# Performance work log

Measured on AMD Instinct MI355X. Metric: run time of the kernel, lower is better.

Reference implementation:

```python
import jax, jax.numpy as jnp
import numpy as np

N = 50000      # nodes
E = 800000     # edges (before self-loops)
F_IN = 256     # feature_size
H = 96         # hidden_channels
G = 64         # graphs in batch
NC = 4         # num_classes
EPS = 1e-5     # BatchNorm eps


def _lrelu(x, s=0.01):
    return jnp.where(x >= 0, x, s * x)


def _gat(x, W, a_s, a_d, b, src, dst):
    # PyG GATConv, heads=1: linear transform, edge-wise LeakyReLU(0.2) scores,
    # segment softmax over destination nodes, scatter-add aggregation.
    h = x @ W                                                  # [N,H]
    e = _lrelu((h * a_s).sum(-1)[src] + (h * a_d).sum(-1)[dst], 0.2)  # [E+N]
    m = jax.ops.segment_max(e, dst, num_segments=N)
    ee = jnp.exp(e - m[dst])
    denom = jax.ops.segment_sum(ee, dst, num_segments=N)
    alpha = ee / denom[dst]
    return jax.ops.segment_sum(alpha[:, None] * h[src], dst, num_segments=N) + b


def _bn(x, g, b):
    # training-mode BatchNorm over the node dimension
    mu = x.mean(0)
    var = ((x - mu) ** 2).mean(0)
    return g * (x - mu) / jnp.sqrt(var + EPS) + b


def setup_inputs() -> dict:
    key = jax.random.key(0)
    ks = jax.random.split(key, 20)
    p = lambda i, sh: jax.random.normal(ks[i], sh, jnp.float32) * 0.05
    inp = {
        "x": jax.random.normal(ks[0], (N, F_IN), jnp.float32),
        "edge_index": jax.random.randint(ks[1], (2, E), 0, N),
        "batch": jnp.sort(jax.random.randint(ks[2], (N,), 0, G)),
        "embed_W": p(3, (F_IN, H)), "embed_b": jnp.zeros((H,), jnp.float32),
        "conv1_W": p(4, (H, H)), "conv1_as": p(5, (H,)), "conv1_ad": p(6, (H,)), "conv1_b": jnp.zeros((H,), jnp.float32),
        "conv2_W": p(7, (H, H)), "conv2_as": p(8, (H,)), "conv2_ad": p(9, (H,)), "conv2_b": jnp.zeros((H,), jnp.float32),
        "conv3_W": p(10, (H, H)), "conv3_as": p(11, (H,)), "conv3_ad": p(12, (H,)), "conv3_b": jnp.zeros((H,), jnp.float32),
        "fc1_W": p(13, (H, H)), "fc1_b": jnp.zeros((H,), jnp.float32),
        "fc2_W": p(14, (H, H)), "fc2_b": jnp.zeros((H,), jnp.float32),
        "bn1_g": jnp.ones((H,), jnp.float32), "bn1_b": jnp.zeros((H,), jnp.float32),
        "bn2_g": jnp.ones((H,), jnp.float32), "bn2_b": jnp.zeros((H,), jnp.float32),
        "bn3_g": jnp.ones((H,), jnp.float32), "bn3_b": jnp.zeros((H,), jnp.float32),
        "fc3_W": p(15, (H, H // 2)), "fc3_b": jnp.zeros((H // 2,), jnp.float32),
        "fc4_W": p(16, (H // 2, NC)), "fc4_b": jnp.zeros((NC,), jnp.float32),
    }
    return inp


def reference(x, edge_index, batch, embed_W, embed_b,
              conv1_W, conv1_as, conv1_ad, conv1_b,
              conv2_W, conv2_as, conv2_ad, conv2_b,
              conv3_W, conv3_as, conv3_ad, conv3_b,
              fc1_W, fc1_b, fc2_W, fc2_b,
              bn1_g, bn1_b, bn2_g, bn2_b, bn3_g, bn3_b,
              fc3_W, fc3_b, fc4_W, fc4_b):
    loops = jnp.arange(N)
    src = jnp.concatenate([edge_index[0], loops])   # GATConv add_self_loops=True
    dst = jnp.concatenate([edge_index[1], loops])

    h = _lrelu(x @ embed_W + embed_b)
    identity = h
    h = _lrelu(_bn(_gat(h, conv1_W, conv1_as, conv1_ad, conv1_b, src, dst), bn1_g, bn1_b)) + identity
    h = _lrelu(h @ fc1_W + fc1_b)
    h = _lrelu(_bn(_gat(h, conv2_W, conv2_as, conv2_ad, conv2_b, src, dst), bn2_g, bn2_b)) + identity
    h = _lrelu(h @ fc2_W + fc2_b)
    h = _lrelu(_bn(_gat(h, conv3_W, conv3_as, conv3_ad, conv3_b, src, dst), bn3_g, bn3_b)) + identity

    # Poincare ball expmap0 with c=1: tanh(||u||) * u / ||u||
    n = jnp.maximum(jnp.linalg.norm(h, axis=-1, keepdims=True), 1e-15)
    h = jnp.tanh(n) * h / n

    cnt = jax.ops.segment_sum(jnp.ones((N,), h.dtype), batch, num_segments=G)
    pooled = jax.ops.segment_sum(h, batch, num_segments=G) / jnp.maximum(cnt, 1.0)[:, None]

    o = _lrelu(pooled @ fc3_W + fc3_b)
    return o @ fc4_W + fc4_b
```

## Files before the change

kernel.cpp:

```cpp
#include <hip/hip_runtime.h>
#include <hip/hip_bf16.h>

#define DEVINL __device__ __forceinline__

constexpr int N_NODES = 50000;
constexpr int N_EDGES = 800000;
constexpr int F_IN    = 256;
constexpr int H       = 96;
constexpr int NG      = 64;
constexpr float BN_EPS = 1e-5f;
constexpr int SLOT    = 64;
constexpr int NREP    = 8;
constexpr int REPSZ   = NG * H + NG;

typedef short bf16x8 __attribute__((ext_vector_type(8)));
typedef float f32x4  __attribute__((ext_vector_type(4)));

DEVINL float bf2f(unsigned int u) {
    union { unsigned int i; float f; } c; c.i = u << 16; return c.f;
}
DEVINL unsigned short f2bf(float f) {
    union { float f; unsigned int i; } c; c.f = f;
    unsigned int x = c.i;
    return (unsigned short)((x + 0x7fffu + ((x >> 16) & 1u)) >> 16);
}
DEVINL float lrelu01(float v) { return v >= 0.f ? v : 0.01f * v; }
DEVINL float ldf(const void* p, size_t i, int f32) {
    return f32 ? ((const float*)p)[i] : bf2f(((const unsigned short*)p)[i]);
}

__global__ __launch_bounds__(256) void detect_fill_k(const unsigned short* __restrict__ x,
                                                     int* __restrict__ flag,
                                                     int* __restrict__ fill)
{
    if (blockIdx.x == 0 && threadIdx.x < 64) {
        int l = threadIdx.x;
        float f = bf2f(x[l]);
        bool huge = !(fabsf(f) <= 1e4f);
        unsigned long long m = __ballot(huge);
        if (l == 0) flag[0] = (__popcll(m) >= 8) ? 1 : 0;
    }
    int i = blockIdx.x * 256 + threadIdx.x;
    if (i < N_NODES) fill[i] = 0;
}

__global__ __launch_bounds__(256) void wpackall_k(
    const void* __restrict__ sE, const void* __restrict__ s0,
    const void* __restrict__ s1, const void* __restrict__ s2,
    const void* __restrict__ s3, const void* __restrict__ s4,
    const int* __restrict__ dflag,
    unsigned short* __restrict__ dE, unsigned short* __restrict__ d0,
    unsigned short* __restrict__ d1, unsigned short* __restrict__ d2,
    unsigned short* __restrict__ d3, unsigned short* __restrict__ d4)
{
    int b = blockIdx.x;
    const void* src; unsigned short* dst; int K, i0;
    if (b < 96) { src = sE; dst = dE; K = F_IN; i0 = b * 256; }
    else {
        int m = (b - 96) / 36, r = (b - 96) % 36;
        K = H; i0 = r * 256;
        if      (m == 0) { src = s0; dst = d0; }
        else if (m == 1) { src = s1; dst = d1; }
        else if (m == 2) { src = s2; dst = d2; }
        else if (m == 3) { src = s3; dst = d3; }
        else             { src = s4; dst = d4; }
    }
    int i = i0 + threadIdx.x;
    if (i >= K * 96) return;
    int c   = i / 3072;
    int rem = i - c * 3072;
    int t    = rem >> 9;
    int rem2 = rem & 511;
    int l = rem2 >> 3, j = rem2 & 7;
    int k = c * 32 + (l >> 4) * 8 + j;
    int n = t * 16 + (l & 15);
    if (dflag[0]) dst[i] = f2bf(((const float*)src)[k * 96 + n]);
    else          dst[i] = ((const unsigned short*)src)[k * 96 + n];
}

template<int EPI, int AWS, int SD, int ABN, int SCAT>
__global__ __launch_bounds__(256) void mgemm_k(
    const void* __restrict__ Ap, const unsigned short* __restrict__ Wpk,
    const void* __restrict__ bp, const int* __restrict__ dflag,
    unsigned short* __restrict__ out, unsigned short* __restrict__ out2,
    const void* __restrict__ as_, const void* __restrict__ ad_,
    float* __restrict__ s, float* __restrict__ d,
    const float* __restrict__ coefp, const unsigned short* __restrict__ idn,
    const int* __restrict__ ei, int* __restrict__ fill,
    unsigned short* __restrict__ colw, int e0, int e1, int ngb,
    int M, int K)
{
    if (SCAT && (int)blockIdx.x >= ngb) {
        int e = e0 + ((int)blockIdx.x - ngb) * 256 + threadIdx.x;
        if (e < e1) {
            int srcv = ei[e];
            int dstv = ei[N_EDGES + e];
            int p = atomicAdd(&fill[dstv], 1);
            if (p < SLOT) colw[(size_t)dstv * SLOT + p] = (unsigned short)srcv;
        }
        return;
    }

    const int f32  = AWS ? 0 : dflag[0];
    const int wf32 = dflag[0];
    const int l    = threadIdx.x & 63;
    const int wave = threadIdx.x >> 6;
    const int row0 = blockIdx.x * 64 + wave * 16;
    const int m    = l & 15;
    const int q    = l >> 4;
    const int arow = row0 + m;
    const bool aok = arow < M;

    f32x4 acc[6] = {};
    const int nch = K >> 5;
    const bf16x8* wp = (const bf16x8*)Wpk;

    for (int c = 0; c < nch; c++) {
        bf16x8 a = {};
        if (aok) {
            if (ABN) {
                const int f0 = c * 32 + q * 8;
                uint4 xu = *(const uint4*)((const unsigned short*)Ap + (size_t)arow * K + f0);
                uint4 iu = *(const uint4*)(idn + (size_t)arow * K + f0);
                unsigned int xs[4] = { xu.x, xu.y, xu.z, xu.w };
                unsigned int is[4] = { iu.x, iu.y, iu.z, iu.w };
                #pragma unroll
                for (int jj = 0; jj < 4; jj++) {
                    int f = f0 + 2 * jj;
                    float v0 = lrelu01(bf2f(xs[jj] & 0xffff) * coefp[f]     + coefp[96 + f])     + bf2f(is[jj] & 0xffff);
                    float v1 = lrelu01(bf2f(xs[jj] >> 16)    * coefp[f + 1] + coefp[96 + f + 1]) + bf2f(is[jj] >> 16);
                    a[2 * jj]     = (short)f2bf(v0);
                    a[2 * jj + 1] = (short)f2bf(v1);
                }
            } else if (f32) {
                const float* A = (const float*)Ap + (size_t)arow * K + c * 32 + q * 8;
                #pragma unroll
                for (int j = 0; j < 8; j++) a[j] = (short)f2bf(A[j]);
            } else {
                a = *(const bf16x8*)((const unsigned short*)Ap + (size_t)arow * K + c * 32 + q * 8);
            }
        }
        const int base = c * 384 + l;
        #pragma unroll
        for (int t = 0; t < 6; t++)
            acc[t] = __builtin_amdgcn_mfma_f32_16x16x32_bf16(a, wp[base + t * 64], acc[t], 0, 0, 0);
    }

    float bv[6];
    if (EPI > 0) {
        #pragma unroll
        for (int t = 0; t < 6; t++) bv[t] = ldf(bp, t * 16 + m, wf32);
    }
    #pragma unroll
    for (int r = 0; r < 4; r++) {
        int rr = row0 + q * 4 + r;
        if (rr >= M) continue;
        size_t o = (size_t)rr * 96 + m;
        #pragma unroll
        for (int t = 0; t < 6; t++) {
            float v = acc[t][r];
            if (EPI > 0) v = lrelu01(v + bv[t]);
            unsigned short sv = f2bf(v);
            out[o + t * 16] = sv;
            if (EPI == 2) out2[o + t * 16] = sv;
        }
    }

    if (SD) {
        float asv[6], adv[6];
        #pragma unroll
        for (int t = 0; t < 6; t++) {
            asv[t] = ldf(as_, t * 16 + m, wf32);
            adv[t] = ldf(ad_, t * 16 + m, wf32);
        }
        #pragma unroll
        for (int r = 0; r < 4; r++) {
            float ps = 0.f, pd = 0.f;
            #pragma unroll
            for (int t = 0; t < 6; t++) {
                ps = fmaf(acc[t][r], asv[t], ps);
                pd = fmaf(acc[t][r], adv[t], pd);
            }
            #pragma unroll
            for (int off = 1; off < 16; off <<= 1) {
                ps += __shfl_xor(ps, off);
                pd += __shfl_xor(pd, off);
            }
            int rr = row0 + q * 4 + r;
            if (m == 0 && rr < M) { s[rr] = ps; d[rr] = pd; }
        }
    }
}

__global__ __launch_bounds__(256) void agg_k(
    const unsigned short* __restrict__ h2, const float* __restrict__ s,
    const float* __restrict__ d, const int* __restrict__ fill,
    const unsigned short* __restrict__ col, const void* __restrict__ bias,
    const int* __restrict__ dflag, unsigned short* __restrict__ out,
    float* __restrict__ bnsum, float* __restrict__ zp, int M)
{
    __shared__ uint2 uwb[4][80];
    if (blockIdx.x == 0 && threadIdx.x < 192) bnsum[threadIdx.x] = 0.f;
    if (zp) {
        int zi = blockIdx.x * 256 + threadIdx.x;
        if (zi < NREP * REPSZ) zp[zi] = 0.f;
    }
    int f32 = dflag[0];
    int v = (blockIdx.x * blockDim.x + threadIdx.x) >> 6;
    int l = threadIdx.x & 63;
    int wv = threadIdx.x >> 6;
    if (v >= M) return;
    int st   = v * SLOT;
    int degr = min(fill[v], SLOT - 1);
    int deg  = degr + 1;

    float dv = d[v];
    int u = 0; float e = -1e30f;
    if (l < degr) {
        u = col[st + l];
        float t = s[u] + dv;
        e = t >= 0.f ? t : 0.2f * t;
    } else if (l == degr) {
        u = v;
        float t = s[v] + dv;
        e = t >= 0.f ? t : 0.2f * t;
    }
    float lm = e;
    #pragma unroll
    for (int off = 32; off > 0; off >>= 1) lm = fmaxf(lm, __shfl_xor(lm, off));
    float w = (l < deg) ? __expf(e - lm) : 0.f;
    float ls = w;
    #pragma unroll
    for (int off = 32; off > 0; off >>= 1) ls += __shfl_xor(ls, off);
    float rden = 1.0f / ls;

    uwb[wv][l] = make_uint2((unsigned int)u, __float_as_uint(w));
    if (l < 16) uwb[wv][64 + l] = make_uint2(0u, 0u);

    bool hw = (l < 48);
    int  c2 = 2 * l;
    float a0 = 0.f, a1 = 0.f;
    const uint2* myuw = uwb[wv];
    for (int j = 0; j < deg; j += 16) {
        uint2 p[16];
        #pragma unroll
        for (int k = 0; k < 16; k++) p[k] = myuw[j + k];
        if (hw) {
            unsigned int hv[16];
            #pragma unroll
            for (int k = 0; k < 16; k++)
                hv[k] = *(const unsigned int*)(h2 + (size_t)p[k].x * 96 + c2);
            #pragma unroll
            for (int k = 0; k < 16; k++) {
                float wj = __uint_as_float(p[k].y);
                a0 = fmaf(wj, bf2f(hv[k] & 0xffff), a0);
                a1 = fmaf(wj, bf2f(hv[k] >> 16),    a1);
            }
        }
    }
    if (hw) {
        float b0 = ldf(bias, c2,     f32);
        float b1 = ldf(bias, c2 + 1, f32);
        unsigned int o = (unsigned int)f2bf(a0 * rden + b0)
                       | ((unsigned int)f2bf(a1 * rden + b1) << 16);
        *(unsigned int*)(out + (size_t)v * 96 + c2) = o;
    }
}

__global__ __launch_bounds__(192) void bnstats_k(const unsigned short* __restrict__ x,
                                                 float* __restrict__ sums, int M)
{
    int c  = threadIdx.x % 96;
    int g2 = threadIdx.x / 96;
    float s = 0.f, q = 0.f;
    for (int r = blockIdx.x * 2 + g2; r < M; r += gridDim.x * 2) {
        float v = bf2f(x[(size_t)r * 96 + c]);
        s += v; q += v * v;
    }
    __shared__ float lsd[192], lqd[192];
    lsd[threadIdx.x] = s; lqd[threadIdx.x] = q;
    __syncthreads();
    if (g2 == 0) {
        atomicAdd(&sums[c],      s + lsd[threadIdx.x + 96]);
        atomicAdd(&sums[96 + c], q + lqd[threadIdx.x + 96]);
    }
}

__global__ void bncoef_k(const float* __restrict__ sums,
                         const void* __restrict__ g_,
                         const void* __restrict__ b_,
                         const int* __restrict__ dflag,
                         float* __restrict__ coef)
{
    int c = threadIdx.x;
    if (c >= 96) return;
    int f32 = dflag[0];
    float mu  = sums[c] * (1.f / N_NODES);
    float var = sums[96 + c] * (1.f / N_NODES) - mu * mu;
    float rinv = 1.0f / sqrtf(var + BN_EPS);
    float sc = ldf(g_, c, f32) * rinv;
    coef[c]      = sc;
    coef[96 + c] = ldf(b_, c, f32) - mu * sc;
}

__global__ __launch_bounds__(256) void bnpool_k(
    const unsigned short* __restrict__ h, const float* __restrict__ coef,
    const unsigned short* __restrict__ iden, const int* __restrict__ batch,
    float* __restrict__ pooled8, int M)
{
    int w = (blockIdx.x * blockDim.x + threadIdx.x) >> 6;
    int l = threadIdx.x & 63;
    int v0 = w * 16;
    if (v0 >= M) return;
    float* P = pooled8 + (blockIdx.x & (NREP - 1)) * REPSZ;
    float* C = P + NG * H;
    bool hw = (l < 48);
    int  c2 = 2 * l;
    float sc0 = 0.f, sc1 = 0.f, sh0 = 0.f, sh1 = 0.f;
    if (hw) {
        sc0 = coef[c2]; sc1 = coef[c2 + 1];
        sh0 = coef[96 + c2]; sh1 = coef[97 + c2];
    }
    int nv = min(16, M - v0);

    int gb[16];
    #pragma unroll
    for (int k = 0; k < 16; k++) gb[k] = batch[v0 + min(k, nv - 1)];

    float x0[16], x1[16], q[16];
    #pragma unroll
    for (int k = 0; k < 16; k++) { x0[k] = 0.f; x1[k] = 0.f; q[k] = 0.f; }
    if (hw) {
        unsigned int xu[16], iu[16];
        #pragma unroll
        for (int k = 0; k < 16; k++) {
            int v = v0 + k;
            if (k < nv) {
                xu[k] = *(const unsigned int*)(h    + (size_t)v * 96 + c2);
                iu[k] = *(const unsigned int*)(iden + (size_t)v * 96 + c2);
            } else { xu[k] = 0u; iu[k] = 0u; }
        }
        #pragma unroll
        for (int k = 0; k < 16; k++) {
            x0[k] = lrelu01(bf2f(xu[k] & 0xffff) * sc0 + sh0) + bf2f(iu[k] & 0xffff);
            x1[k] = lrelu01(bf2f(xu[k] >> 16)    * sc1 + sh1) + bf2f(iu[k] >> 16);
            q[k]  = x0[k] * x0[k] + x1[k] * x1[k];
        }
    }

    #pragma unroll
    for (int off = 32; off > 0; off >>= 1) {
        #pragma unroll
        for (int k = 0; k < 16; k++) q[k] += __shfl_xor(q[k], off);
    }

    float f[16];
    #pragma unroll
    for (int k = 0; k < 16; k++) {
        float n = fmaxf(sqrtf(q[k]), 1e-15f);
        if (n < 15.f) {
            float t = __expf(2.f * n);
            f[k] = (t - 1.f) / ((t + 1.f) * n);
        } else {
            f[k] = 1.f / n;
        }
    }

    float a0 = 0.f, a1 = 0.f, cnt = 0.f;
    int curg = -1;
    for (int k = 0; k < nv; k++) {
        int g = gb[k];
        if (g != curg) {
            if (curg >= 0) {
                if (hw) {
                    atomicAdd(&P[curg * 96 + c2],     a0);
                    atomicAdd(&P[curg * 96 + c2 + 1], a1);
                }
                if (l == 0) atomicAdd(&C[curg], cnt);
            }
            a0 = a1 = 0.f; cnt = 0.f; curg = g;
        }
        a0 = fmaf(f[k], x0[k], a0);
        a1 = fmaf(f[k], x1[k], a1);
        cnt += 1.f;
    }
    if (curg >= 0) {
        if (hw) {
            atomicAdd(&P[curg * 96 + c2],     a0);
            atomicAdd(&P[curg * 96 + c2 + 1], a1);
        }
        if (l == 0) atomicAdd(&C[curg], cnt);
    }
}

__global__ __launch_bounds__(64) void head_k(const float* __restrict__ pooled8,
                                             const void* __restrict__ w3,
                                             const void* __restrict__ b3,
                                             const void* __restrict__ w4,
                                             const void* __restrict__ b4,
                                             const int* __restrict__ dflag,
                                             void* __restrict__ outv)
{
    int g = blockIdx.x;
    int t = threadIdx.x;
    int f32 = dflag[0];
    __shared__ float p[96];
    __shared__ float o[48];
    float cs = 0.f;
    #pragma unroll
    for (int r = 0; r < NREP; r++) cs += pooled8[r * REPSZ + NG * H + g];
    float inv = 1.0f / fmaxf(cs, 1.0f);
    for (int c = t; c < 96; c += 64) {
        float v = 0.f;
        #pragma unroll
        for (int r = 0; r < NREP; r++) v += pooled8[r * REPSZ + g * 96 + c];
        p[c] = v * inv;
    }
    __syncthreads();
    if (t < 48) {
        float a = ldf(b3, t, f32);
        #pragma unroll
        for (int c = 0; c < 96; c++) a = fmaf(p[c], ldf(w3, (size_t)c * 48 + t, f32), a);
        o[t] = lrelu01(a);
    }
    __syncthreads();
    if (t < 4) {
        float a = ldf(b4, t, f32);
        #pragma unroll
        for (int j = 0; j < 48; j++) a = fmaf(o[j], ldf(w4, j * 4 + t, f32), a);
        if (f32) ((float*)outv)[g * 4 + t] = a;
        else     ((unsigned short*)outv)[g * 4 + t] = f2bf(a);
    }
}

extern "C" void kernel_launch(void* const* d_in, const int* in_sizes, int n_in,
                              void* d_out, int out_size, void* d_ws, size_t ws_size,
                              hipStream_t stream)
{
    const void* x     = d_in[0];
    const int*  ei    = (const int*)d_in[1];
    const int*  batch = (const int*)d_in[2];
    const void* embW  = d_in[3];
    const void* embB  = d_in[4];
    const void* convW[3]  = { d_in[5],  d_in[9],  d_in[13] };
    const void* convAs[3] = { d_in[6],  d_in[10], d_in[14] };
    const void* convAd[3] = { d_in[7],  d_in[11], d_in[15] };
    const void* convB[3]  = { d_in[8],  d_in[12], d_in[16] };
    const void* fcW[2]    = { d_in[17], d_in[19] };
    const void* fcB[2]    = { d_in[18], d_in[20] };
    const void* bnG[3]    = { d_in[21], d_in[23], d_in[25] };
    const void* bnB[3]    = { d_in[22], d_in[24], d_in[26] };
    const void* fc3W = d_in[27];
    const void* fc3b = d_in[28];
    const void* fc4W = d_in[29];
    const void* fc4b = d_in[30];

    char* wp_ = (char*)d_ws;
    auto alloc = [&](size_t b) { char* p = wp_; wp_ += (b + 255) & ~(size_t)255; return p; };
    int*   dflag = (int*)alloc(256);
    unsigned short* ident = (unsigned short*)alloc((size_t)N_NODES * H * 2);
    unsigned short* hA    = (unsigned short*)alloc((size_t)N_NODES * H * 2);
    unsigned short* hB    = (unsigned short*)alloc((size_t)N_NODES * H * 2);
    float* s_sc  = (float*)alloc((size_t)N_NODES * 4);
    float* d_sc  = (float*)alloc((size_t)N_NODES * 4);
    float* bnsum = (float*)alloc(192 * 4);
    float* coef  = (float*)alloc(192 * 4);
    float* pooled8 = (float*)alloc((size_t)NREP * REPSZ * 4);
    int*   fill  = (int*)alloc((size_t)N_NODES * 4);
    unsigned short* col = (unsigned short*)alloc((size_t)N_NODES * SLOT * 2);
    unsigned short* wpkEmb = (unsigned short*)alloc((size_t)F_IN * 96 * 2);
    unsigned short* wpkS[5];
    for (int i = 0; i < 5; i++) wpkS[i] = (unsigned short*)alloc((size_t)H * 96 * 2);

    const int GM = (N_NODES + 63) / 64;
    const int GW = (N_NODES * 64 + 255) / 256;
    const int GP = ((N_NODES + 15) / 16 * 64 + 255) / 256;
    const int GF = (N_NODES + 255) / 256;
    const int EH = N_EDGES / 2;
    const int GS = (EH + 255) / 256;

    detect_fill_k<<<GF, 256, 0, stream>>>((const unsigned short*)x, dflag, fill);

    wpackall_k<<<276, 256, 0, stream>>>(embW, convW[0], convW[1], convW[2], fcW[0], fcW[1],
                                        dflag, wpkEmb, wpkS[0], wpkS[1], wpkS[2], wpkS[3], wpkS[4]);

    mgemm_k<2, 0, 0, 0, 1><<<GM + GS, 256, 0, stream>>>(
        x, wpkEmb, embB, dflag, hA, ident,
        nullptr, nullptr, nullptr, nullptr, nullptr, nullptr,
        ei, fill, col, 0, EH, GM, N_NODES, F_IN);

    unsigned short* hcur = hA;
    unsigned short* htmp = hB;

    for (int l = 0; l < 3; l++) {
        if (l == 0) {
            mgemm_k<0, 1, 1, 0, 1><<<GM + GS, 256, 0, stream>>>(
                hcur, wpkS[0], nullptr, dflag, htmp, nullptr,
                convAs[0], convAd[0], s_sc, d_sc, nullptr, nullptr,
                ei, fill, col, EH, N_EDGES, GM, N_NODES, H);
        } else {
            mgemm_k<0, 1, 1, 0, 0><<<GM, 256, 0, stream>>>(
                hcur, wpkS[l], nullptr, dflag, htmp, nullptr,
                convAs[l], convAd[l], s_sc, d_sc, nullptr, nullptr,
                nullptr, nullptr, nullptr, 0, 0, GM, N_NODES, H);
        }
        agg_k<<<GW, 256, 0, stream>>>(htmp, s_sc, d_sc, fill, col, convB[l], dflag, hcur,
                                      bnsum, (l == 2) ? pooled8 : nullptr, N_NODES);
        bnstats_k<<<512, 192, 0, stream>>>(hcur, bnsum, N_NODES);
        bncoef_k<<<1, 128, 0, stream>>>(bnsum, bnG[l], bnB[l], dflag, coef);
        if (l < 2) {
            mgemm_k<1, 1, 0, 1, 0><<<GM, 256, 0, stream>>>(
                hcur, wpkS[3 + l], fcB[l], dflag, htmp, nullptr,
                nullptr, nullptr, nullptr, nullptr, coef, ident,
                nullptr, nullptr, nullptr, 0, 0, GM, N_NODES, H);
            unsigned short* t = hcur; hcur = htmp; htmp = t;
        }
    }

    bnpool_k<<<GP, 256, 0, stream>>>(hcur, coef, ident, batch, pooled8, N_NODES);
    head_k<<<NG, 64, 0, stream>>>(pooled8, fc3W, fc3b, fc4W, fc4b, dflag, d_out);
}
```

Baseline: 438.0 us.

## Replicate CSR fill counters across 8 copies to cut atomic contention, merge later

Edge bucketing by destination now runs entirely inside the embedding GEMM launch and spreads its atomics over 8 replicated counter/slot arrays, picked by block index. The conv1 GEMM launch then gets extra blocks that compact the 8 per-replica slot lists into the single 64-slot column list via wave shuffles. The aim is to reduce atomic contention on the shared fill counters. In exchange it adds memory traffic and a compaction step, and per-replica slots are capped at 24, which can drop edges for high-degree nodes.

```diff
diff --git a/kernel.cpp b/kernel.cpp
--- a/kernel.cpp
+++ b/kernel.cpp
@@ -10,6 +10,7 @@
 constexpr int NG      = 64;
 constexpr float BN_EPS = 1e-5f;
 constexpr int SLOT    = 64;
+constexpr int SLOT8   = 24;
 constexpr int NREP    = 8;
 constexpr int REPSZ   = NG * H + NG;
 
@@ -31,7 +32,7 @@
 
 __global__ __launch_bounds__(256) void detect_fill_k(const unsigned short* __restrict__ x,
                                                      int* __restrict__ flag,
-                                                     int* __restrict__ fill)
+                                                     int* __restrict__ fill8)
 {
     if (blockIdx.x == 0 && threadIdx.x < 64) {
         int l = threadIdx.x;
@@ -41,7 +42,7 @@
         if (l == 0) flag[0] = (__popcll(m) >= 8) ? 1 : 0;
     }
     int i = blockIdx.x * 256 + threadIdx.x;
-    if (i < N_NODES) fill[i] = 0;
+    if (i < NREP * N_NODES) fill8[i] = 0;
 }
 
 __global__ __launch_bounds__(256) void wpackall_k(
@@ -86,17 +87,41 @@
     const void* __restrict__ as_, const void* __restrict__ ad_,
     float* __restrict__ s, float* __restrict__ d,
     const float* __restrict__ coefp, const unsigned short* __restrict__ idn,
-    const int* __restrict__ ei, int* __restrict__ fill,
-    unsigned short* __restrict__ colw, int e0, int e1, int ngb,
+    const int* __restrict__ ei, int* __restrict__ fill8,
+    unsigned short* __restrict__ col8, int* __restrict__ fillo,
+    unsigned short* __restrict__ colo, int ngb,
     int M, int K)
 {
-    if (SCAT && (int)blockIdx.x >= ngb) {
-        int e = e0 + ((int)blockIdx.x - ngb) * 256 + threadIdx.x;
-        if (e < e1) {
+    if (SCAT == 1 && (int)blockIdx.x >= ngb) {
+        int e = ((int)blockIdx.x - ngb) * 256 + threadIdx.x;
+        if (e < N_EDGES) {
             int srcv = ei[e];
             int dstv = ei[N_EDGES + e];
-            int p = atomicAdd(&fill[dstv], 1);
-            if (p < SLOT) colw[(size_t)dstv * SLOT + p] = (unsigned short)srcv;
+            int rep  = blockIdx.x & (NREP - 1);
+            int p = atomicAdd(&fill8[(size_t)rep * N_NODES + dstv], 1);
+            if (p < SLOT8) col8[((size_t)rep * N_NODES + dstv) * SLOT8 + p] = (unsigned short)srcv;
+        }
+        return;
+    }
+    if (SCAT == 2 && (int)blockIdx.x >= ngb) {
+        int v = ((int)blockIdx.x - ngb) * 4 + (threadIdx.x >> 6);
+        if (v < N_NODES) {
+            int l = threadIdx.x & 63;
+            int fr = 0;
+            if (l < 8) fr = min(fill8[(size_t)l * N_NODES + v], SLOT8);
+            int c[8];
+            #pragma unroll
+            for (int r = 0; r < 8; r++) c[r] = __shfl(fr, r);
+            int rsel = 0, slot = 0, acc = 0;
+            #pragma unroll
+            for (int rr = 0; rr < 8; rr++) {
+                if (l >= acc && l < acc + c[rr]) { rsel = rr; slot = l - acc; }
+                acc += c[rr];
+            }
+            int total = min(acc, SLOT - 1);
+            if (l < total) colo[(size_t)v * SLOT + l] =
+                col8[((size_t)rsel * N_NODES + v) * SLOT8 + slot];
+            if (l == 0) fillo[v] = total;
         }
         return;
     }
@@ -466,6 +491,8 @@
     float* bnsum = (float*)alloc(192 * 4);
     float* coef  = (float*)alloc(192 * 4);
     float* pooled8 = (float*)alloc((size_t)NREP * REPSZ * 4);
+    int*   fill8 = (int*)alloc((size_t)NREP * N_NODES * 4);
+    unsigned short* col8 = (unsigned short*)alloc((size_t)NREP * N_NODES * SLOT8 * 2);
     int*   fill  = (int*)alloc((size_t)N_NODES * 4);
     unsigned short* col = (unsigned short*)alloc((size_t)N_NODES * SLOT * 2);
     unsigned short* wpkEmb = (unsigned short*)alloc((size_t)F_IN * 96 * 2);
@@ -475,34 +502,34 @@
     const int GM = (N_NODES + 63) / 64;
     const int GW = (N_NODES * 64 + 255) / 256;
     const int GP = ((N_NODES + 15) / 16 * 64 + 255) / 256;
-    const int GF = (N_NODES + 255) / 256;
-    const int EH = N_EDGES / 2;
-    const int GS = (EH + 255) / 256;
-
-    detect_fill_k<<<GF, 256, 0, stream>>>((const unsigned short*)x, dflag, fill);
+    const int GF = (NREP * N_NODES + 255) / 256;
+    const int GSA = (N_EDGES + 255) / 256;
+    const int GMR = (N_NODES + 3) / 4;
+
+    detect_fill_k<<<GF, 256, 0, stream>>>((const unsigned short*)x, dflag, fill8);
 
     wpackall_k<<<276, 256, 0, stream>>>(embW, convW[0], convW[1], convW[2], fcW[0], fcW[1],
                                         dflag, wpkEmb, wpkS[0], wpkS[1], wpkS[2], wpkS[3], wpkS[4]);
 
-    mgemm_k<2, 0, 0, 0, 1><<<GM + GS, 256, 0, stream>>>(
+    mgemm_k<2, 0, 0, 0, 1><<<GM + GSA, 256, 0, stream>>>(
         x, wpkEmb, embB, dflag, hA, ident,
         nullptr, nullptr, nullptr, nullptr, nullptr, nullptr,
-        ei, fill, col, 0, EH, GM, N_NODES, F_IN);
+        ei, fill8, col8, nullptr, nullptr, GM, N_NODES, F_IN);
 
     unsigned short* hcur = hA;
     unsigned short* htmp = hB;
 
     for (int l = 0; l < 3; l++) {
         if (l == 0) {
-            mgemm_k<0, 1, 1, 0, 1><<<GM + GS, 256, 0, stream>>>(
+            mgemm_k<0, 1, 1, 0, 2><<<GM + GMR, 256, 0, stream>>>(
                 hcur, wpkS[0], nullptr, dflag, htmp, nullptr,
                 convAs[0], convAd[0], s_sc, d_sc, nullptr, nullptr,
-                ei, fill, col, EH, N_EDGES, GM, N_NODES, H);
+                nullptr, fill8, col8, fill, col, GM, N_NODES, H);
         } else {
             mgemm_k<0, 1, 1, 0, 0><<<GM, 256, 0, stream>>>(
                 hcur, wpkS[l], nullptr, dflag, htmp, nullptr,
                 convAs[l], convAd[l], s_sc, d_sc, nullptr, nullptr,
-                nullptr, nullptr, nullptr, 0, 0, GM, N_NODES, H);
+                nullptr, nullptr, nullptr, nullptr, nullptr, GM, N_NODES, H);
         }
         agg_k<<<GW, 256, 0, stream>>>(htmp, s_sc, d_sc, fill, col, convB[l], dflag, hcur,
                                       bnsum, (l == 2) ? pooled8 : nullptr, N_NODES);
@@ -512,7 +539,7 @@
             mgemm_k<1, 1, 0, 1, 0><<<GM, 256, 0, stream>>>(
                 hcur, wpkS[3 + l], fcB[l], dflag, htmp, nullptr,
                 nullptr, nullptr, nullptr, nullptr, coef, ident,
-                nullptr, nullptr, nullptr, 0, 0, GM, N_NODES, H);
+                nullptr, nullptr, nullptr, nullptr, nullptr, GM, N_NODES, H);
             unsigned short* t = hcur; hcur = htmp; htmp = t;
         }
     }
```

Result: no change. 443.3 us (+1.2%).
